# Optimization experiments

Hardware: AMD Instinct MI355X
Metric: run time of the kernel (lower is better)

The kernel has to match this reference:

```python
import jax, jax.numpy as jnp
import numpy as np
import math

B, S, D, H, K = 8, 4096, 1024, 16, 256
DK = D // H


def setup_inputs() -> dict:
    key = jax.random.key(0)
    ks = jax.random.split(key, 8)
    s = 1.0 / math.sqrt(D)
    x = jax.random.normal(ks[0], (B, S, D), dtype=jnp.float32)
    Wq = jax.random.normal(ks[1], (D, D), dtype=jnp.float32) * s
    Wk = jax.random.normal(ks[2], (D, D), dtype=jnp.float32) * s
    Wv = jax.random.normal(ks[3], (D, D), dtype=jnp.float32) * s
    Wo = jax.random.normal(ks[4], (D, D), dtype=jnp.float32) * s
    bq = jnp.zeros((D,), jnp.float32)
    bk = jnp.zeros((D,), jnp.float32)
    bv = jnp.zeros((D,), jnp.float32)
    bo = jnp.zeros((D,), jnp.float32)
    # xavier-uniform-style scale for the low-rank projections
    lim = math.sqrt(6.0 / (S + K))
    E = jax.random.uniform(ks[5], (S, K), jnp.float32, -lim, lim)
    Fp = jax.random.uniform(ks[6], (S, K), jnp.float32, -lim, lim)
    return {"x": x, "Wq": Wq, "bq": bq, "Wk": Wk, "bk": bk,
            "Wv": Wv, "bv": bv, "Wo": Wo, "bo": bo, "E": E, "Fp": Fp}


def reference(x, Wq, bq, Wk, bk, Wv, bv, Wo, bo, E, Fp):
    b, s, d = x.shape
    # QKV projections, split heads: [b, h, s, dk]
    def heads(y):
        return y.reshape(b, s, H, DK).transpose(0, 2, 1, 3)
    Q = heads(x @ Wq + bq)
    Kh = heads(x @ Wk + bk)
    Vh = heads(x @ Wv + bv)
    # Low-rank projection of K, V along sequence: [b, h, k, dk]
    Kp = jnp.einsum('sk,bhsd->bhkd', E, Kh)
    Vp = jnp.einsum('sk,bhsd->bhkd', Fp, Vh)
    # Attention over projected length k
    scores = jnp.einsum('bhsd,bhkd->bhsk', Q, Kp) / math.sqrt(DK)
    attn = jax.nn.softmax(scores, axis=-1)
    out = jnp.einsum('bhsk,bhkd->bhsd', attn, Vp)
    out = out.transpose(0, 2, 1, 3).reshape(b, s, d)
    return out @ Wo + bo
```

## Files before the change

### kernel.cpp

```cpp
#include <hip/hip_runtime.h>

#define AS1 __attribute__((address_space(1)))
#define AS3 __attribute__((address_space(3)))

typedef __attribute__((ext_vector_type(8))) short s16x8;
typedef __attribute__((ext_vector_type(4))) float f32x4;
typedef __attribute__((ext_vector_type(4))) unsigned short u16x4;
typedef __attribute__((ext_vector_type(8))) unsigned short u16x8;

#define MFMA16(a, b, c) __builtin_amdgcn_mfma_f32_16x16x32_bf16(a, b, c, 0, 0, 0)

static __device__ __forceinline__ unsigned short f2bf(float f) {
  unsigned u = __builtin_bit_cast(unsigned, f);
  u += 0x7fffu + ((u >> 16) & 1u);
  return (unsigned short)(u >> 16);
}

static __device__ __forceinline__ void gll16(const unsigned short* g, char* l) {
  __builtin_amdgcn_global_load_lds((const AS1 void*)g, (AS3 void*)l, 16, 0, 0);
}

#define BAR() asm volatile("s_barrier" ::: "memory")
#define WAITV(N) asm volatile("s_waitcnt vmcnt(" #N ")" ::: "memory")
#define FENCE() asm volatile("" ::: "memory")

__device__ __forceinline__ void gemm256_pipe(const unsigned short* __restrict__ A0, int lda,
                                             const unsigned short* __restrict__ B0, int ldb,
                                             int NT2, char* lds, f32x4 (&acc)[8][4]) {
  const int t = threadIdx.x;
  const int lane = t & 63, w = t >> 6, g = lane >> 4, l15 = lane & 15;
  const int wm = w >> 2, wn = w & 3;
  char* const A_lds[2] = {lds, lds + 65536};
  char* const B_lds[2] = {lds + 32768, lds + 98304};
  s16x8 af[2][4], bfr[2][4];

  const int rl = t >> 3, sl = t & 7;
  const unsigned short* aB = A0 + (size_t)rl * lda + ((sl ^ (rl & 7)) << 3);
  const unsigned short* bB = B0 + (size_t)rl * ldb + ((sl ^ (rl & 7)) << 3);
  const int woff = w << 10;

  char* pA[2][2];
  char* pB[2][2];
#pragma unroll
  for (int b = 0; b < 2; ++b)
#pragma unroll
    for (int kk = 0; kk < 2; ++kk) {
      pA[b][kk] = lds + b * 65536 + (wm * 64 + l15) * 128 + (((kk * 4 + g) ^ (l15 & 7)) << 4);
      pB[b][kk] = lds + 32768 + b * 65536 + (wn * 32 + l15) * 128 + (((kk * 4 + g) ^ (l15 & 7)) << 4);
    }

#define STGA(BUF, H, PTR)                                                                \
  do {                                                                                   \
    gll16((PTR) + (size_t)((H)*128) * lda, A_lds[BUF] + woff + (H)*16384);               \
    gll16((PTR) + (size_t)((H)*128 + 64) * lda, A_lds[BUF] + woff + (H)*16384 + 8192);   \
  } while (0)
#define STGB(BUF, H, PTR)                                                                \
  do {                                                                                   \
    gll16((PTR) + (size_t)((H)*128) * ldb, B_lds[BUF] + woff + (H)*16384);               \
    gll16((PTR) + (size_t)((H)*128 + 64) * ldb, B_lds[BUF] + woff + (H)*16384 + 8192);   \
  } while (0)

#define LDAQ(BUF, QH)                                                                    \
  do {                                                                                   \
    _Pragma("unroll") for (int mi = 0; mi < 4; ++mi)                                     \
        _Pragma("unroll") for (int kk = 0; kk < 2; ++kk)                                 \
            af[kk][mi] = *(const s16x8*)(pA[BUF][kk] + (QH)*16384 + mi * 2048);          \
  } while (0)
#define LDBP(BUF, NH)                                                                    \
  do {                                                                                   \
    _Pragma("unroll") for (int ni = 0; ni < 2; ++ni)                                     \
        _Pragma("unroll") for (int kk = 0; kk < 2; ++kk)                                 \
            bfr[kk][(NH)*2 + ni] =                                                       \
                *(const s16x8*)(pB[BUF][kk] + (NH)*16384 + ni * 2048);                   \
  } while (0)
#define MQUAD(QH, NH)                                                                    \
  do {                                                                                   \
    __builtin_amdgcn_s_setprio(1);                                                       \
    _Pragma("unroll") for (int kk = 0; kk < 2; ++kk)                                     \
        _Pragma("unroll") for (int mi = 0; mi < 4; ++mi)                                 \
            _Pragma("unroll") for (int ni = 0; ni < 2; ++ni)                             \
                acc[(QH)*4 + mi][(NH)*2 + ni] =                                          \
        MFMA16(af[kk][mi], bfr[kk][(NH)*2 + ni], acc[(QH)*4 + mi][(NH)*2 + ni]);         \
    __builtin_amdgcn_s_setprio(0);                                                       \
  } while (0)

  STGA(0, 0, aB);
  STGB(0, 0, bB);
  STGB(0, 1, bB);
  STGA(0, 1, aB);
  STGA(1, 0, aB + 64);
  STGB(1, 0, bB + 64);
  STGB(1, 1, bB + 64);
  STGA(1, 1, aB + 64);
  WAITV(8);
  BAR();

  for (int it = 0; it < NT2; ++it) {
    const bool pf = (it + 1 < NT2);
    const unsigned short* aN = aB + it * 128 + 128;
    const unsigned short* bN = bB + it * 128 + 128;
    LDAQ(0, 0);
    LDBP(0, 0);
    MQUAD(0, 0);
    BAR();
    LDBP(0, 1);
    if (pf) { STGA(0, 0, aN); STGB(0, 0, bN); }
    MQUAD(0, 1);
    BAR();
    LDAQ(0, 1);
    if (pf) STGB(0, 1, bN);
    MQUAD(1, 0);
    BAR();
    if (pf) STGA(0, 1, aN);
    MQUAD(1, 1);
    if (pf) WAITV(8);
    else WAITV(0);
    BAR();
    LDAQ(1, 0);
    LDBP(1, 0);
    MQUAD(0, 0);
    BAR();
    LDBP(1, 1);
    if (pf) { STGA(1, 0, aN + 64); STGB(1, 0, bN + 64); }
    MQUAD(0, 1);
    BAR();
    LDAQ(1, 1);
    if (pf) STGB(1, 1, bN + 64);
    MQUAD(1, 0);
    BAR();
    if (pf) STGA(1, 1, aN + 64);
    MQUAD(1, 1);
    if (pf) WAITV(8);
    BAR();
  }
#undef STGA
#undef STGB
#undef LDAQ
#undef LDBP
#undef MQUAD
}

__global__ __launch_bounds__(512, 2) void k_gemm_q(const unsigned short* __restrict__ xb,
                                                   const unsigned short* __restrict__ Wqt,
                                                   const float* __restrict__ biasq,
                                                   unsigned short* __restrict__ Qb) {
  __shared__ __align__(16) char lds[131072];
  f32x4 acc[8][4];
#pragma unroll
  for (int i = 0; i < 8; ++i)
#pragma unroll
    for (int j = 0; j < 4; ++j) acc[i][j] = f32x4{0.f, 0.f, 0.f, 0.f};
  int bid = blockIdx.y * 4 + blockIdx.x;
  bid = (bid & 7) * 64 + (bid >> 3);
  const int bn = bid & 3, bm = bid >> 2;
  gemm256_pipe(xb + (size_t)bm * 256 * 1024, 1024, Wqt + (size_t)bn * 256 * 1024, 1024, 8, lds, acc);

  const int t = threadIdx.x, lane = t & 63, w = t >> 6, g = lane >> 4, l15 = lane & 15;
  const int wm = w >> 2, wn = w & 3;
  const float QSC = 0.1803368801111204f;
#pragma unroll
  for (int nf = 0; nf < 4; ++nf) {
    const int n = bn * 256 + (nf >> 1) * 128 + wn * 32 + (nf & 1) * 16 + l15;
    const float bias = biasq[n];
#pragma unroll
    for (int mq = 0; mq < 8; ++mq) {
      const int m0 = bm * 256 + (mq >> 2) * 128 + wm * 64 + (mq & 3) * 16 + g * 4;
      const f32x4 v = acc[mq][nf];
#pragma unroll
      for (int r = 0; r < 4; ++r) Qb[(size_t)(m0 + r) * 1024 + n] = f2bf((v[r] + bias) * QSC);
    }
  }
}

__global__ __launch_bounds__(512, 2) void k_gemm_out(const unsigned short* __restrict__ AO,
                                                     const unsigned short* __restrict__ Wot,
                                                     const float* __restrict__ bo,
                                                     float* __restrict__ out) {
  __shared__ __align__(16) char lds[131072];
  f32x4 acc[8][4];
#pragma unroll
  for (int i = 0; i < 8; ++i)
#pragma unroll
    for (int j = 0; j < 4; ++j) acc[i][j] = f32x4{0.f, 0.f, 0.f, 0.f};
  int bid = blockIdx.y * 4 + blockIdx.x;
  bid = (bid & 7) * 64 + (bid >> 3);
  const int bn = bid & 3, bm = bid >> 2;
  gemm256_pipe(AO + (size_t)bm * 256 * 1024, 1024, Wot + (size_t)bn * 256 * 1024, 1024, 8, lds, acc);

  const int t = threadIdx.x, lane = t & 63, w = t >> 6, g = lane >> 4, l15 = lane & 15;
  const int wm = w >> 2, wn = w & 3;
#pragma unroll
  for (int nf = 0; nf < 4; ++nf) {
    const int n = bn * 256 + (nf >> 1) * 128 + wn * 32 + (nf & 1) * 16 + l15;
    const float bias = bo[n];
#pragma unroll
    for (int mq = 0; mq < 8; ++mq) {
      const int m0 = bm * 256 + (mq >> 2) * 128 + wm * 64 + (mq & 3) * 16 + g * 4;
      const f32x4 v = acc[mq][nf];
#pragma unroll
      for (int r = 0; r < 4; ++r) out[(size_t)(m0 + r) * 1024 + n] = v[r] + bias;
    }
  }
}

__device__ __forceinline__ void gemm_tile(const unsigned short* __restrict__ Ab, int lda,
                                          const unsigned short* __restrict__ Bb, int ldb,
                                          int Kc, char* lds, f32x4 (&acc)[4][4]) {
  const int t = threadIdx.x;
  const int lane = t & 63, w = t >> 6, g = lane >> 4, l15 = lane & 15;
  const int wm = w >> 1, wn = w & 1;
  char* As = lds;
  char* Bs = lds + 16384;
  for (int ks = 0; ks < Kc; ks += 64) {
    __syncthreads();
#pragma unroll
    for (int i = 0; i < 4; ++i) {
      const int c = i * 256 + t, row = c >> 3, sl = c & 7;
      const int col = ks + ((sl ^ (row & 7)) << 3);
      const int ubase = (i * 256 + w * 64) << 4;
      gll16(Ab + (size_t)row * lda + col, As + ubase);
      gll16(Bb + (size_t)row * ldb + col, Bs + ubase);
    }
    __syncthreads();
    s16x8 af[2][4], bfr[2][4];
#pragma unroll
    for (int kk = 0; kk < 2; ++kk)
#pragma unroll
      for (int x4 = 0; x4 < 4; ++x4) {
        const int ra = wm * 64 + x4 * 16 + l15;
        const int rb = wn * 64 + x4 * 16 + l15;
        af[kk][x4] = *(const s16x8*)(As + ra * 128 + ((((kk << 2) + g) ^ (ra & 7)) << 4));
        bfr[kk][x4] = *(const s16x8*)(Bs + rb * 128 + ((((kk << 2) + g) ^ (rb & 7)) << 4));
      }
#pragma unroll
    for (int kk = 0; kk < 2; ++kk)
#pragma unroll
      for (int mt = 0; mt < 4; ++mt)
#pragma unroll
        for (int nt = 0; nt < 4; ++nt)
          acc[mt][nt] = MFMA16(af[kk][mt], bfr[kk][nt], acc[mt][nt]);
  }
}

__global__ __launch_bounds__(256) void k_gemm_xef(const unsigned short* __restrict__ Et,
                                                  const unsigned short* __restrict__ Ft,
                                                  const unsigned short* __restrict__ xbT,
                                                  float* __restrict__ pxef) {
  __shared__ __align__(16) char lds[32768];
  f32x4 acc[4][4];
#pragma unroll
  for (int i = 0; i < 4; ++i)
#pragma unroll
    for (int j = 0; j < 4; ++j) acc[i][j] = f32x4{0.f, 0.f, 0.f, 0.f};
  const int z = blockIdx.z;
  const int ks = z >> 4, pair = z & 15, b = pair >> 1, ef = pair & 1;
  const unsigned short* Ab = (ef ? Ft : Et) + blockIdx.y * 128 * 4096 + ks * 1024;
  const unsigned short* Bb = xbT + (size_t)b * 4194304 + blockIdx.x * 128 * 4096 + ks * 1024;
  gemm_tile(Ab, 4096, Bb, 4096, 1024, lds, acc);

  const int t = threadIdx.x, lane = t & 63, w = t >> 6, g = lane >> 4, l15 = lane & 15;
  const int wm = w >> 1, wn = w & 1;
  const int nb = blockIdx.x * 128 + wn * 64, mb = blockIdx.y * 128 + wm * 64;
  float* C = pxef + (size_t)z * 262144;
#pragma unroll
  for (int nt = 0; nt < 4; ++nt) {
    const int n = nb + nt * 16 + l15;
#pragma unroll
    for (int mt = 0; mt < 4; ++mt) {
      const int m0 = mb + mt * 16 + g * 4;
      const f32x4 v = acc[mt][nt];
#pragma unroll
      for (int r = 0; r < 4; ++r) C[(m0 + r) * 1024 + n] = v[r];
    }
  }
}

__global__ __launch_bounds__(256) void k_xef_red(const float* __restrict__ pxef,
                                                 unsigned short* __restrict__ xEF) {
  const int j = (blockIdx.x * 256 + threadIdx.x) * 4;
  f32x4 s = *(const f32x4*)(pxef + j);
#pragma unroll
  for (int ks = 1; ks < 4; ++ks) {
    const f32x4 p = *(const f32x4*)(pxef + (size_t)ks * 4194304 + j);
#pragma unroll
    for (int r = 0; r < 4; ++r) s[r] += p[r];
  }
  u16x4 o;
#pragma unroll
  for (int r = 0; r < 4; ++r) o[r] = f2bf(s[r]);
  *(u16x4*)(xEF + j) = o;
}

__global__ __launch_bounds__(256) void k_kpvp2(const unsigned short* __restrict__ xEF,
                                               const unsigned short* __restrict__ Wqkvt,
                                               const float* __restrict__ biasq,
                                               const float* __restrict__ sEF,
                                               unsigned short* __restrict__ Kp,
                                               unsigned short* __restrict__ VpT) {
  __shared__ __align__(16) char lds[32768];
  f32x4 acc[4][4];
#pragma unroll
  for (int i = 0; i < 4; ++i)
#pragma unroll
    for (int j = 0; j < 4; ++j) acc[i][j] = f32x4{0.f, 0.f, 0.f, 0.f};
  const int b = blockIdx.z >> 1, kv = blockIdx.z & 1;
  const unsigned short* Ab = xEF + (size_t)(b * 2 + kv) * 262144 + blockIdx.y * 128 * 1024;
  const unsigned short* Bb = Wqkvt + (size_t)(1 + kv) * 1048576 + blockIdx.x * 128 * 1024;
  gemm_tile(Ab, 1024, Bb, 1024, 1024, lds, acc);

  const int t = threadIdx.x, lane = t & 63, w = t >> 6, g = lane >> 4, l15 = lane & 15;
  const int wm = w >> 1, wn = w & 1;
  const int nb = blockIdx.x * 128 + wn * 64, mb = blockIdx.y * 128 + wm * 64;
  const float* bias = biasq + (1 + kv) * 1024;
  const float* sE = sEF + kv * 256;
  if (!kv) {
    unsigned short* C = Kp + b * 262144;
#pragma unroll
    for (int nt = 0; nt < 4; ++nt) {
      const int n = nb + nt * 16 + l15;
      const float bn_ = bias[n];
#pragma unroll
      for (int mt = 0; mt < 4; ++mt) {
        const int m0 = mb + mt * 16 + g * 4;
        const f32x4 v = acc[mt][nt];
#pragma unroll
        for (int r = 0; r < 4; ++r) C[(m0 + r) * 1024 + n] = f2bf(v[r] + sE[m0 + r] * bn_);
      }
    }
  } else {
    unsigned short* C = VpT + b * 262144;
#pragma unroll
    for (int nt = 0; nt < 4; ++nt) {
      const int n = nb + nt * 16 + l15;
      const float bn_ = bias[n];
#pragma unroll
      for (int mt = 0; mt < 4; ++mt) {
        const int m0 = mb + mt * 16 + g * 4;
        const f32x4 v = acc[mt][nt];
        u16x4 pk;
#pragma unroll
        for (int r = 0; r < 4; ++r) pk[r] = f2bf(v[r] + sE[m0 + r] * bn_);
        *(u16x4*)(C + (n << 8) + m0) = pk;
      }
    }
  }
}

__global__ __launch_bounds__(512, 2) void k_attn(const unsigned short* __restrict__ Qb,
                                                 const unsigned short* __restrict__ Kp,
                                                 const unsigned short* __restrict__ VpT,
                                                 unsigned short* __restrict__ AO) {
  __shared__ __align__(16) char lds[131072];
  char* K0 = lds;
  char* V0 = lds + 32768;
  char* Qd = lds + 65536;
  char* Pb = lds + 98304;
  const int t = threadIdx.x, lane = t & 63, w = t >> 6, g = lane >> 4, l15 = lane & 15;
  const int sh = blockIdx.x, h = blockIdx.y, b = blockIdx.z;
  const int s0 = sh * 2048;
  const unsigned short* Qg = Qb + (size_t)(b * 4096 + s0) * 1024 + h * 64;
  const unsigned short* Kg = Kp + b * 262144 + h * 64;
  const unsigned short* Vg = VpT + b * 262144 + (h * 64) * 256;

#pragma unroll
  for (int i = 0; i < 4; ++i) {
    const int c = i * 512 + t, row = c >> 3, slr = c & 7;
    gll16(Kg + row * 1024 + ((slr ^ (row & 7)) << 3), K0 + ((i * 512 + w * 64) << 4));
  }
#pragma unroll
  for (int i = 0; i < 4; ++i) {
    const int c = i * 512 + t, row = c >> 5, slr = c & 31;
    gll16(Vg + row * 256 + ((slr ^ (row & 7)) << 3), V0 + ((i * 512 + w * 64) << 4));
  }
#pragma unroll
  for (int i = 0; i < 2; ++i) {
    const int c = i * 512 + t, row = c >> 3, slr = c & 7;
    gll16(Qg + row * 1024 + ((slr ^ (row & 7)) << 3), Qd + ((i * 512 + w * 64) << 4));
  }
  __syncthreads();

  char* const PwRow = Pb + (w << 12) + l15 * 256;
  const int wOffP = (g * 8 + l15 * 16) & 255;
  const int qrow = w * 16 + l15;
  const int qsw0 = (g ^ (qrow & 7)) << 4;
  const int qsw1 = ((4 + g) ^ (qrow & 7)) << 4;

  for (int st = 0; st < 16; ++st) {
    char* qb = Qd + ((st & 1) << 14);
    const s16x8 aq0 = *(const s16x8*)(qb + qrow * 128 + qsw0);
    const s16x8 aq1 = *(const s16x8*)(qb + qrow * 128 + qsw1);
    if (st < 15) {
      const unsigned short* Qn = Qg + (size_t)(st + 1) * 131072;
      char* qn = Qd + (((st + 1) & 1) << 14);
#pragma unroll
      for (int i = 0; i < 2; ++i) {
        const int c = i * 512 + t, row = c >> 3, slr = c & 7;
        gll16(Qn + row * 1024 + ((slr ^ (row & 7)) << 3), qn + ((i * 512 + w * 64) << 4));
      }
    }

    f32x4 sc[16];
#pragma unroll
    for (int nt = 0; nt < 16; ++nt) sc[nt] = f32x4{0.f, 0.f, 0.f, 0.f};
#pragma unroll
    for (int nt = 0; nt < 16; ++nt) {
      const int row = nt * 16 + l15;
      const s16x8 b0 = *(const s16x8*)(K0 + row * 128 + ((g ^ (row & 7)) << 4));
      const s16x8 b1 = *(const s16x8*)(K0 + row * 128 + (((4 + g) ^ (row & 7)) << 4));
      sc[nt] = MFMA16(b0, aq0, sc[nt]);
      sc[nt] = MFMA16(b1, aq1, sc[nt]);
    }

    float sm_ = 0.f;
    f32x4 ov[4];
#pragma unroll
    for (int nt = 0; nt < 4; ++nt) ov[nt] = f32x4{0.f, 0.f, 0.f, 0.f};

#pragma unroll
    for (int half = 0; half < 2; ++half) {
#pragma unroll
      for (int nt2 = 0; nt2 < 8; ++nt2) {
        const f32x4 s4 = sc[half * 8 + nt2];
        const float p0 = __builtin_amdgcn_exp2f(s4[0]);
        const float p1 = __builtin_amdgcn_exp2f(s4[1]);
        const float p2 = __builtin_amdgcn_exp2f(s4[2]);
        const float p3 = __builtin_amdgcn_exp2f(s4[3]);
        sm_ += (p0 + p1) + (p2 + p3);
        u16x4 pk;
        pk[0] = f2bf(p0);
        pk[1] = f2bf(p1);
        pk[2] = f2bf(p2);
        pk[3] = f2bf(p3);
        *(u16x4*)(PwRow + ((nt2 * 32 + wOffP) & 255)) = pk;
      }
      FENCE();
#pragma unroll
      for (int kk = 0; kk < 4; ++kk) {
        const int slh = ((kk * 4 + g + l15) & 15) << 4;
        const s16x8 ap = *(const s16x8*)(PwRow + slh);
#pragma unroll
        for (int nt = 0; nt < 4; ++nt) {
          const int rv = nt * 16 + l15;
          const int slot = half * 16 + (kk << 2) + g;
          const s16x8 bv = *(const s16x8*)(V0 + rv * 512 + ((slot ^ (rv & 7)) << 4));
          ov[nt] = MFMA16(ap, bv, ov[nt]);
        }
      }
      FENCE();
    }
    sm_ += __shfl_xor(sm_, 16);
    sm_ += __shfl_xor(sm_, 32);
    const float inv = 1.f / sm_;
    float invr[4];
#pragma unroll
    for (int r = 0; r < 4; ++r) invr[r] = __shfl(inv, (g << 2) + r);

    unsigned short* Ao = AO + (size_t)(b * 4096 + s0 + st * 128 + w * 16) * 1024 + h * 64;
#pragma unroll
    for (int nt = 0; nt < 4; ++nt) {
#pragma unroll
      for (int r = 0; r < 4; ++r) {
        Ao[(g * 4 + r) * 1024 + nt * 16 + l15] = f2bf(ov[nt][r] * invr[r]);
      }
    }
    __syncthreads();
  }
}

__global__ __launch_bounds__(256) void k_cvt_xt(const float* __restrict__ x,
                                                unsigned short* __restrict__ xb,
                                                unsigned short* __restrict__ xbT) {
  __shared__ unsigned short tl[256 * 72];
  const int t = threadIdx.x;
  const int stile = blockIdx.x >> 4, dt = blockIdx.x & 15;
  const int s0 = stile * 256, d0 = dt * 64;
  const int q = t >> 4, l15 = t & 15;

#pragma unroll
  for (int p = 0; p < 16; ++p) {
    const int row = p * 16 + q;
    const float4 v = *(const float4*)(x + (size_t)(s0 + row) * 1024 + d0 + l15 * 4);
    u16x4 o;
    o[0] = f2bf(v.x);
    o[1] = f2bf(v.y);
    o[2] = f2bf(v.z);
    o[3] = f2bf(v.w);
    *(u16x4*)(xb + (size_t)(s0 + row) * 1024 + d0 + l15 * 4) = o;
    *(u16x4*)(tl + row * 72 + ((l15 ^ p) << 2)) = o;
  }
  __syncthreads();

  u16x4 in[16];
#pragma unroll
  for (int i = 0; i < 16; ++i) {
    const int s = l15 * 16 + i;
    in[i] = *(const u16x4*)(tl + s * 72 + ((q ^ l15) << 2));
  }
  const int b = s0 >> 12, sb = s0 & 4095;
#pragma unroll
  for (int j = 0; j < 4; ++j) {
    u16x8 o0, o1;
#pragma unroll
    for (int i = 0; i < 8; ++i) {
      o0[i] = in[i][j];
      o1[i] = in[8 + i][j];
    }
    unsigned short* dst = xbT + (size_t)b * 4194304 + (size_t)(d0 + q * 4 + j) * 4096 + sb + l15 * 16;
    *(u16x8*)dst = o0;
    *(u16x8*)(dst + 8) = o1;
  }
}

__global__ __launch_bounds__(256) void k_colsum1(const float* __restrict__ E,
                                                 const float* __restrict__ Fp,
                                                 float* __restrict__ part) {
  const int sc = blockIdx.x, ef = blockIdx.y, k = threadIdx.x;
  const float* M = ef ? Fp : E;
  float s = 0.f;
#pragma unroll 4
  for (int i = 0; i < 256; ++i) s += M[(size_t)((sc << 8) + i) * 256 + k];
  part[(ef * 16 + sc) * 256 + k] = s;
}

__global__ __launch_bounds__(256) void k_prep(const float* __restrict__ Wq, const float* __restrict__ Wk,
                                              const float* __restrict__ Wv, const float* __restrict__ Wo,
                                              const float* __restrict__ E, const float* __restrict__ Fp,
                                              const float* __restrict__ bq, const float* __restrict__ bk,
                                              const float* __restrict__ bv,
                                              const float* __restrict__ part,
                                              unsigned short* __restrict__ Wqkvt, unsigned short* __restrict__ Wot,
                                              unsigned short* __restrict__ Et, unsigned short* __restrict__ Ft,
                                              float* __restrict__ biasq, float* __restrict__ sEF) {
  const int i = blockIdx.x * 256 + threadIdx.x;
  if (i < 3145728) {
    const int gsel = i >> 20, rem = i & 1048575, n = rem >> 10, k = rem & 1023;
    const float* W = gsel == 0 ? Wq : (gsel == 1 ? Wk : Wv);
    Wqkvt[i] = f2bf(W[(k << 10) + n]);
  } else if (i < 4194304) {
    const int j = i - 3145728, n = j >> 10, k = j & 1023;
    Wot[j] = f2bf(Wo[(k << 10) + n]);
  } else if (i < 5242880) {
    const int j = i - 4194304, kp = j >> 12, s = j & 4095;
    Et[j] = f2bf(E[(s << 8) + kp]);
  } else if (i < 6291456) {
    const int j = i - 5242880, kp = j >> 12, s = j & 4095;
    Ft[j] = f2bf(Fp[(s << 8) + kp]);
  } else if (i < 6294528) {
    const int j = i - 6291456;
    biasq[j] = (j < 1024) ? bq[j] : (j < 2048 ? bk[j - 1024] : bv[j - 2048]);
  } else if (i < 6295040) {
    const int j = i - 6294528;
    const int ef = j >> 8, k = j & 255;
    float s = 0.f;
#pragma unroll
    for (int c = 0; c < 16; ++c) s += part[(ef * 16 + c) * 256 + k];
    sEF[j] = s;
  }
}

extern "C" void kernel_launch(void* const* d_in, const int* in_sizes, int n_in,
                              void* d_out, int out_size, void* d_ws, size_t ws_size,
                              hipStream_t stream) {
  const float* x = (const float*)d_in[0];
  const float* Wq = (const float*)d_in[1];
  const float* bq = (const float*)d_in[2];
  const float* Wk = (const float*)d_in[3];
  const float* bk = (const float*)d_in[4];
  const float* Wv = (const float*)d_in[5];
  const float* bv = (const float*)d_in[6];
  const float* Wo = (const float*)d_in[7];
  const float* bo = (const float*)d_in[8];
  const float* E = (const float*)d_in[9];
  const float* Fp = (const float*)d_in[10];

  char* ws = (char*)d_ws;
  size_t off = 0;
  auto alloc = [&](size_t bytes) {
    char* p = ws + off;
    off += (bytes + 255) & ~(size_t)255;
    return p;
  };
  unsigned short* xb = (unsigned short*)alloc(33554432ull * 2);
  unsigned short* xbT = (unsigned short*)alloc(33554432ull * 2);
  unsigned short* Qb = (unsigned short*)alloc(33554432ull * 2);
  unsigned short* Wqkvt = (unsigned short*)alloc(3145728ull * 2);
  unsigned short* Wot = (unsigned short*)alloc(1048576ull * 2);
  unsigned short* Et = (unsigned short*)alloc(1048576ull * 2);
  unsigned short* Ft = (unsigned short*)alloc(1048576ull * 2);
  unsigned short* xEF = (unsigned short*)alloc(4194304ull * 2);
  unsigned short* Kp = (unsigned short*)alloc(2097152ull * 2);
  unsigned short* VpT = (unsigned short*)alloc(2097152ull * 2);
  float* pxef = (float*)alloc(16777216ull * 4);
  float* biasq = (float*)alloc(3072 * 4);
  float* part = (float*)alloc(8192 * 4);
  float* sEF = (float*)alloc(512 * 4);
  (void)in_sizes; (void)n_in; (void)out_size; (void)ws_size;

  k_cvt_xt<<<2048, 256, 0, stream>>>(x, xb, xbT);
  k_colsum1<<<dim3(16, 2), 256, 0, stream>>>(E, Fp, part);
  k_prep<<<24590, 256, 0, stream>>>(Wq, Wk, Wv, Wo, E, Fp, bq, bk, bv, part,
                                    Wqkvt, Wot, Et, Ft, biasq, sEF);
  k_gemm_q<<<dim3(4, 128), 512, 0, stream>>>(xb, Wqkvt, biasq, Qb);
  k_gemm_xef<<<dim3(8, 2, 64), 256, 0, stream>>>(Et, Ft, xbT, pxef);
  k_xef_red<<<4096, 256, 0, stream>>>(pxef, xEF);
  k_kpvp2<<<dim3(8, 2, 16), 256, 0, stream>>>(xEF, Wqkvt, biasq, sEF, Kp, VpT);
  k_attn<<<dim3(2, 16, 8), 512, 0, stream>>>(Qb, Kp, VpT, xb);
  k_gemm_out<<<dim3(4, 128), 512, 0, stream>>>(xb, Wot, bo, (float*)d_out);
}
```

Measured before the change: 422.9 us.

## Double-buffer A fragments to overlap LDS reads with MFMA in GEMM pipeline

Splits the A-fragment registers into two sets so LDS reads for the next quadrant are issued before the current quadrant's MFMAs run. The GEMM main loop is reordered into a software-pipelined schedule, with explicit lgkmcnt waits before the global-to-LDS stores and adjusted vmcnt waits. The aim is to hide LDS read latency behind matrix-core work. The cost is higher VGPR pressure and finer-grained hazard management across barriers, which could hurt occupancy or correctness if any wait count is wrong.

```diff
diff --git a/kernel.cpp b/kernel.cpp
--- a/kernel.cpp
+++ b/kernel.cpp
@@ -22,6 +22,7 @@
 
 #define BAR() asm volatile("s_barrier" ::: "memory")
 #define WAITV(N) asm volatile("s_waitcnt vmcnt(" #N ")" ::: "memory")
+#define WAITLG(N) asm volatile("s_waitcnt lgkmcnt(" #N ")" ::: "memory")
 #define FENCE() asm volatile("" ::: "memory")
 
 __device__ __forceinline__ void gemm256_pipe(const unsigned short* __restrict__ A0, int lda,
@@ -32,7 +33,7 @@
   const int wm = w >> 2, wn = w & 3;
   char* const A_lds[2] = {lds, lds + 65536};
   char* const B_lds[2] = {lds + 32768, lds + 98304};
-  s16x8 af[2][4], bfr[2][4];
+  s16x8 af0[2][4], af1[2][4], bfr[2][4];
 
   const int rl = t >> 3, sl = t & 7;
   const unsigned short* aB = A0 + (size_t)rl * lda + ((sl ^ (rl & 7)) << 3);
@@ -60,27 +61,26 @@
     gll16((PTR) + (size_t)((H)*128 + 64) * ldb, B_lds[BUF] + woff + (H)*16384 + 8192);   \
   } while (0)
 
-#define LDAQ(BUF, QH)                                                                    \
+#define LDAK(DST, BUF, QH, KK)                                                           \
   do {                                                                                   \
     _Pragma("unroll") for (int mi = 0; mi < 4; ++mi)                                     \
-        _Pragma("unroll") for (int kk = 0; kk < 2; ++kk)                                 \
-            af[kk][mi] = *(const s16x8*)(pA[BUF][kk] + (QH)*16384 + mi * 2048);          \
+        DST[KK][mi] = *(const s16x8*)(pA[BUF][KK] + (QH)*16384 + mi * 2048);             \
   } while (0)
-#define LDBP(BUF, NH)                                                                    \
+#define LDBH(BUF, NH)                                                                    \
   do {                                                                                   \
     _Pragma("unroll") for (int ni = 0; ni < 2; ++ni)                                     \
         _Pragma("unroll") for (int kk = 0; kk < 2; ++kk)                                 \
             bfr[kk][(NH)*2 + ni] =                                                       \
                 *(const s16x8*)(pB[BUF][kk] + (NH)*16384 + ni * 2048);                   \
   } while (0)
-#define MQUAD(QH, NH)                                                                    \
+#define MQUAD(AF, QH, NH)                                                                \
   do {                                                                                   \
     __builtin_amdgcn_s_setprio(1);                                                       \
     _Pragma("unroll") for (int kk = 0; kk < 2; ++kk)                                     \
         _Pragma("unroll") for (int mi = 0; mi < 4; ++mi)                                 \
             _Pragma("unroll") for (int ni = 0; ni < 2; ++ni)                             \
                 acc[(QH)*4 + mi][(NH)*2 + ni] =                                          \
-        MFMA16(af[kk][mi], bfr[kk][(NH)*2 + ni], acc[(QH)*4 + mi][(NH)*2 + ni]);         \
+        MFMA16(AF[kk][mi], bfr[kk][(NH)*2 + ni], acc[(QH)*4 + mi][(NH)*2 + ni]);         \
     __builtin_amdgcn_s_setprio(0);                                                       \
   } while (0)
 
@@ -94,49 +94,65 @@
   STGA(1, 1, aB + 64);
   WAITV(8);
   BAR();
+  LDAK(af0, 0, 0, 0);
+  LDBH(0, 0);
 
   for (int it = 0; it < NT2; ++it) {
     const bool pf = (it + 1 < NT2);
     const unsigned short* aN = aB + it * 128 + 128;
     const unsigned short* bN = bB + it * 128 + 128;
-    LDAQ(0, 0);
-    LDBP(0, 0);
-    MQUAD(0, 0);
-    BAR();
-    LDBP(0, 1);
+    LDAK(af0, 0, 0, 1);
+    LDBH(0, 1);
+    MQUAD(af0, 0, 0);
+    BAR();
+    LDAK(af1, 0, 1, 0);
+    MQUAD(af0, 0, 1);
+    WAITLG(4);
     if (pf) { STGA(0, 0, aN); STGB(0, 0, bN); }
-    MQUAD(0, 1);
-    BAR();
-    LDAQ(0, 1);
+    BAR();
+    LDAK(af1, 0, 1, 1);
+    MQUAD(af1, 1, 0);
+    WAITLG(4);
     if (pf) STGB(0, 1, bN);
-    MQUAD(1, 0);
-    BAR();
+    if (pf) WAITV(6);
+    else WAITV(0);
+    BAR();
+    LDAK(af0, 1, 0, 0);
+    LDBH(1, 0);
+    MQUAD(af1, 1, 1);
+    WAITLG(8);
     if (pf) STGA(0, 1, aN);
-    MQUAD(1, 1);
-    if (pf) WAITV(8);
-    else WAITV(0);
-    BAR();
-    LDAQ(1, 0);
-    LDBP(1, 0);
-    MQUAD(0, 0);
-    BAR();
-    LDBP(1, 1);
+    BAR();
+    LDAK(af0, 1, 0, 1);
+    LDBH(1, 1);
+    MQUAD(af0, 0, 0);
+    BAR();
+    LDAK(af1, 1, 1, 0);
+    MQUAD(af0, 0, 1);
+    WAITLG(4);
     if (pf) { STGA(1, 0, aN + 64); STGB(1, 0, bN + 64); }
-    MQUAD(0, 1);
-    BAR();
-    LDAQ(1, 1);
+    BAR();
+    LDAK(af1, 1, 1, 1);
+    MQUAD(af1, 1, 0);
+    WAITLG(4);
     if (pf) STGB(1, 1, bN + 64);
-    MQUAD(1, 0);
-    BAR();
-    if (pf) STGA(1, 1, aN + 64);
-    MQUAD(1, 1);
-    if (pf) WAITV(8);
+    if (pf) WAITV(6);
+    BAR();
+    if (pf) {
+      LDAK(af0, 0, 0, 0);
+      LDBH(0, 0);
+    }
+    MQUAD(af1, 1, 1);
+    if (pf) {
+      WAITLG(8);
+      STGA(1, 1, aN + 64);
+    }
     BAR();
   }
 #undef STGA
 #undef STGB
-#undef LDAQ
-#undef LDBP
+#undef LDAK
+#undef LDBH
 #undef MQUAD
 }
 
```

Result: no change. 427.5 us (+1.1%).

## Tile weight transposes through LDS and fold column sums into the convert kernel

Applied to the files above, without the earlier changes.

The per-element strided transpose-and-convert of Wq/Wk/Wv/Wo/E/Fp in k_prep becomes a 256x64 tiled transpose through shared memory, with coalesced float4 reads and 16-byte writes. The k_colsum1 launch is merged into k_cvt_xt as 32 extra blocks, removing one kernel launch. The previous version read the source matrices with a large stride, so most of each cache line went unused. The tiled version spends more LDS and registers per block.

```diff
diff --git a/kernel.cpp b/kernel.cpp
--- a/kernel.cpp
+++ b/kernel.cpp
@@ -469,7 +469,20 @@
 
 __global__ __launch_bounds__(256) void k_cvt_xt(const float* __restrict__ x,
                                                 unsigned short* __restrict__ xb,
-                                                unsigned short* __restrict__ xbT) {
+                                                unsigned short* __restrict__ xbT,
+                                                const float* __restrict__ E,
+                                                const float* __restrict__ Fp,
+                                                float* __restrict__ part) {
+  if (blockIdx.x >= 2048) {
+    const int bb = blockIdx.x - 2048;
+    const int sc = bb & 15, ef = bb >> 4, k = threadIdx.x;
+    const float* M = ef ? Fp : E;
+    float s = 0.f;
+#pragma unroll 4
+    for (int i = 0; i < 256; ++i) s += M[(size_t)((sc << 8) + i) * 256 + k];
+    part[(ef * 16 + sc) * 256 + k] = s;
+    return;
+  }
   __shared__ unsigned short tl[256 * 72];
   const int t = threadIdx.x;
   const int stile = blockIdx.x >> 4, dt = blockIdx.x & 15;
@@ -511,17 +524,6 @@
   }
 }
 
-__global__ __launch_bounds__(256) void k_colsum1(const float* __restrict__ E,
-                                                 const float* __restrict__ Fp,
-                                                 float* __restrict__ part) {
-  const int sc = blockIdx.x, ef = blockIdx.y, k = threadIdx.x;
-  const float* M = ef ? Fp : E;
-  float s = 0.f;
-#pragma unroll 4
-  for (int i = 0; i < 256; ++i) s += M[(size_t)((sc << 8) + i) * 256 + k];
-  part[(ef * 16 + sc) * 256 + k] = s;
-}
-
 __global__ __launch_bounds__(256) void k_prep(const float* __restrict__ Wq, const float* __restrict__ Wk,
                                               const float* __restrict__ Wv, const float* __restrict__ Wo,
                                               const float* __restrict__ E, const float* __restrict__ Fp,
@@ -531,30 +533,72 @@
                                               unsigned short* __restrict__ Wqkvt, unsigned short* __restrict__ Wot,
                                               unsigned short* __restrict__ Et, unsigned short* __restrict__ Ft,
                                               float* __restrict__ biasq, float* __restrict__ sEF) {
-  const int i = blockIdx.x * 256 + threadIdx.x;
-  if (i < 3145728) {
-    const int gsel = i >> 20, rem = i & 1048575, n = rem >> 10, k = rem & 1023;
-    const float* W = gsel == 0 ? Wq : (gsel == 1 ? Wk : Wv);
-    Wqkvt[i] = f2bf(W[(k << 10) + n]);
-  } else if (i < 4194304) {
-    const int j = i - 3145728, n = j >> 10, k = j & 1023;
-    Wot[j] = f2bf(Wo[(k << 10) + n]);
-  } else if (i < 5242880) {
-    const int j = i - 4194304, kp = j >> 12, s = j & 4095;
-    Et[j] = f2bf(E[(s << 8) + kp]);
-  } else if (i < 6291456) {
-    const int j = i - 5242880, kp = j >> 12, s = j & 4095;
-    Ft[j] = f2bf(Fp[(s << 8) + kp]);
-  } else if (i < 6294528) {
-    const int j = i - 6291456;
-    biasq[j] = (j < 1024) ? bq[j] : (j < 2048 ? bk[j - 1024] : bv[j - 2048]);
-  } else if (i < 6295040) {
-    const int j = i - 6294528;
-    const int ef = j >> 8, k = j & 255;
-    float s = 0.f;
-#pragma unroll
-    for (int c = 0; c < 16; ++c) s += part[(ef * 16 + c) * 256 + k];
-    sEF[j] = s;
+  __shared__ unsigned short tl[256 * 72];
+  const int bid = blockIdx.x, t = threadIdx.x;
+  if (bid >= 384) {
+    if (bid < 396) {
+      const int j = (bid - 384) * 256 + t;
+      biasq[j] = (j < 1024) ? bq[j] : (j < 2048 ? bk[j - 1024] : bv[j - 2048]);
+    } else {
+      const int j = (bid - 396) * 256 + t;
+      const int ef = j >> 8, k = j & 255;
+      float s = 0.f;
+#pragma unroll
+      for (int c = 0; c < 16; ++c) s += part[(ef * 16 + c) * 256 + k];
+      sEF[j] = s;
+    }
+    return;
+  }
+  const float* src;
+  unsigned short* dst;
+  int srcld, dstld, s0, d0;
+  if (bid < 256) {
+    const int m = bid >> 6, tile = bid & 63;
+    src = (m == 0) ? Wq : (m == 1) ? Wk : (m == 2) ? Wv : Wo;
+    dst = (m < 3) ? (Wqkvt + m * 1048576) : Wot;
+    srcld = 1024;
+    dstld = 1024;
+    s0 = (tile >> 4) * 256;
+    d0 = (tile & 15) * 64;
+  } else {
+    const int j = bid - 256, ef = j >> 6, tile = j & 63;
+    src = ef ? Fp : E;
+    dst = ef ? Ft : Et;
+    srcld = 256;
+    dstld = 4096;
+    s0 = (tile >> 2) * 256;
+    d0 = (tile & 3) * 64;
+  }
+  const int q = t >> 4, l15 = t & 15;
+#pragma unroll
+  for (int p = 0; p < 16; ++p) {
+    const int row = p * 16 + q;
+    const float4 v = *(const float4*)(src + (size_t)(s0 + row) * srcld + d0 + l15 * 4);
+    u16x4 o;
+    o[0] = f2bf(v.x);
+    o[1] = f2bf(v.y);
+    o[2] = f2bf(v.z);
+    o[3] = f2bf(v.w);
+    *(u16x4*)(tl + row * 72 + ((l15 ^ p) << 2)) = o;
+  }
+  __syncthreads();
+  u16x4 in[16];
+#pragma unroll
+  for (int i = 0; i < 16; ++i) {
+    const int s = l15 * 16 + i;
+    in[i] = *(const u16x4*)(tl + s * 72 + ((q ^ l15) << 2));
+  }
+#pragma unroll
+  for (int j = 0; j < 4; ++j) {
+    u16x8 o0, o1;
+#pragma unroll
+    for (int i = 0; i < 8; ++i) {
+      o0[i] = in[i][j];
+      o1[i] = in[8 + i][j];
+    }
+    unsigned short* dp = dst + (size_t)(d0 + q * 4 + j) * dstld + s0 + l15 * 16;
+    *(u16x8*)dp = o0;
+    *(u16x8*)(dp + 8) = o1;
   }
 }
 
@@ -596,10 +640,9 @@
   float* sEF = (float*)alloc(512 * 4);
   (void)in_sizes; (void)n_in; (void)out_size; (void)ws_size;
 
-  k_cvt_xt<<<2048, 256, 0, stream>>>(x, xb, xbT);
-  k_colsum1<<<dim3(16, 2), 256, 0, stream>>>(E, Fp, part);
-  k_prep<<<24590, 256, 0, stream>>>(Wq, Wk, Wv, Wo, E, Fp, bq, bk, bv, part,
-                                    Wqkvt, Wot, Et, Ft, biasq, sEF);
+  k_cvt_xt<<<2080, 256, 0, stream>>>(x, xb, xbT, E, Fp, part);
+  k_prep<<<398, 256, 0, stream>>>(Wq, Wk, Wv, Wo, E, Fp, bq, bk, bv, part,
+                                  Wqkvt, Wot, Et, Ft, biasq, sEF);
   k_gemm_q<<<dim3(4, 128), 512, 0, stream>>>(xb, Wqkvt, biasq, Qb);
   k_gemm_xef<<<dim3(8, 2, 64), 256, 0, stream>>>(Et, Ft, xbT, pxef);
   k_xef_red<<<4096, 256, 0, stream>>>(pxef, xEF);
```

New measurement: 400.8 us. 1.06x faster.
